# Kernel optimization log

Hardware: AMD Instinct MI355X
Metric: run time of the kernel (lower is better)

## Reference

```python
import jax, jax.numpy as jnp
import numpy as np

D_MODEL, D_STATE, EXPAND = 1024, 16, 2
D_INNER = EXPAND * D_MODEL
BATCH, SEQ = 4, 4096


def setup_inputs() -> dict:
    key = jax.random.key(0)
    ks = jax.random.split(key, 9)
    s = 0.02
    return {
        "x": jax.random.normal(ks[0], (BATCH, SEQ, D_MODEL), jnp.float32),
        # torch Linear weight [out,in] stored transposed here as [in,out]
        "W_in": jax.random.normal(ks[1], (D_MODEL, 2 * D_INNER), jnp.float32) * s,
        "conv_w": jax.random.normal(ks[2], (D_INNER, 1, 3), jnp.float32) * s,  # depthwise, groups=D_INNER
        "conv_b": jax.random.normal(ks[3], (D_INNER,), jnp.float32) * s,
        "W_B": jax.random.normal(ks[4], (D_INNER, D_STATE), jnp.float32) * s,
        "W_C": jax.random.normal(ks[5], (D_INNER, D_STATE), jnp.float32) * s,
        "A": jax.random.normal(ks[6], (D_STATE,), jnp.float32),
        "D": jnp.ones((D_INNER,), jnp.float32),
        "W_out": jax.random.normal(ks[7], (D_INNER, D_MODEL), jnp.float32) * s,
    }


def reference(x, W_in, conv_w, conv_b, W_B, W_C, A, D, W_out):
    d_inner = conv_w.shape[0]
    # input projection and split into main / residual gate paths
    xr = jnp.einsum("bld,de->ble", x, W_in)  # [B, L, 2*d_inner]
    x_main, res = xr[..., :d_inner], xr[..., d_inner:]
    # depthwise conv1d along seq (kernel 3, pad 1)
    xc = jax.lax.conv_general_dilated(
        x_main.transpose(0, 2, 1), conv_w, (1,), [(1, 1)],
        dimension_numbers=("NCH", "OIH", "NCH"), feature_group_count=d_inner)
    xc = (xc + conv_b[None, :, None]).transpose(0, 2, 1)  # [B, L, d_inner]
    xc = jax.nn.silu(xc)
    # selective-scan inputs
    Bt = jnp.einsum("bli,is->bls", xc, W_B)  # [B, L, d_state]
    Ct = jnp.einsum("bli,is->bls", xc, W_C)
    decay = jnp.exp(-jax.nn.softplus(A))  # exp(A_diag), [d_state]

    def step(state, bc):
        b_t, c_t = bc
        state = state * decay + b_t  # i=0: zeros*decay + B[0] == B[0]
        return state, jnp.sum(state * c_t, axis=-1)  # scalar per batch

    _, ys = jax.lax.scan(step, jnp.zeros_like(Bt[:, 0]),
                         (Bt.transpose(1, 0, 2), Ct.transpose(1, 0, 2)))
    ys = ys.T  # [B, L]
    y = ys[..., None] + xc * D  # broadcast scan output across d_inner
    y = y * jax.nn.silu(res)
    return jnp.einsum("bli,id->bld", y, W_out)
```

## Files before the change

kernel.cpp:

```cpp
#include <hip/hip_runtime.h>


typedef _Float16 half8 __attribute__((ext_vector_type(8)));
typedef float floatx4 __attribute__((ext_vector_type(4)));

#define D_MODEL 1024
#define D_INNER 2048
#define SEQ     4096
#define NBATCH  4
#define NROWS   (NBATCH * SEQ)
#define CHUNK   16
#define NCHUNK  (SEQ / CHUNK)
#define NTASK   (NBATCH * NCHUNK)

__device__ __forceinline__ void async16(_Float16* lds, const _Float16* g) {
    __builtin_amdgcn_global_load_lds((const __attribute__((address_space(1))) void*)g,
                                     (__attribute__((address_space(3))) void*)lds, 16, 0, 0);
}

__device__ __forceinline__ float siluf(float x) {
    return x / (1.f + __expf(-x));
}

__device__ __forceinline__ float decay_of(const float* A, int s) {
    return __expf(-log1pf(__expf(A[s])));
}

#define BAR() asm volatile("s_barrier" ::: "memory")


__global__ __launch_bounds__(256) void convert_f32_f16(const float* __restrict__ src,
                                                       _Float16* __restrict__ dst) {
    size_t idx = ((size_t)blockIdx.x * 256 + threadIdx.x) * 8;
    float4 a = *(const float4*)(src + idx);
    float4 b = *(const float4*)(src + idx + 4);
    half8 o = {(_Float16)a.x, (_Float16)a.y, (_Float16)a.z, (_Float16)a.w,
               (_Float16)b.x, (_Float16)b.y, (_Float16)b.z, (_Float16)b.w};
    *(half8*)(dst + idx) = o;
}

__global__ __launch_bounds__(256) void transpose_to_f16(const float* __restrict__ src,
                                                        _Float16* __restrict__ dst,
                                                        int K, int N) {
    __shared__ float tile[32][33];
    int n0 = blockIdx.x * 32, k0 = blockIdx.y * 32;
    int x = threadIdx.x, y = threadIdx.y;
#pragma unroll
    for (int r = 0; r < 32; r += 8)
        tile[y + r][x] = src[(size_t)(k0 + y + r) * N + (n0 + x)];
    __syncthreads();
#pragma unroll
    for (int r = 0; r < 32; r += 8)
        dst[(size_t)(n0 + y + r) * K + (k0 + x)] = (_Float16)tile[x][y + r];
}

__global__ __launch_bounds__(256) void convert_wbct(const float* __restrict__ WB,
                                                    const float* __restrict__ WC,
                                                    _Float16* __restrict__ WBCT) {
    int idx = blockIdx.x * 256 + threadIdx.x;
    int n = idx >> 11, k = idx & 2047;
    float v = (n < 16) ? WB[k * 16 + n] : WC[k * 16 + (n - 16)];
    WBCT[idx] = (_Float16)v;
}


__device__ __forceinline__ void stage_half(const _Float16* __restrict__ src, int K,
                                           int rowBase, int k0, _Float16* ldsHalf) {
    const int tid = threadIdx.x;
    const int sr = tid >> 3, wid = tid >> 6;
    const int lc = ((tid & 7) ^ (sr & 7)) << 3;
#pragma unroll
    for (int r = 0; r < 2; r++) {
        const _Float16* g = src + (size_t)(rowBase + r * 64 + sr) * K + (k0 + lc);
        async16(ldsHalf + r * 4096 + wid * 512, g);
    }
}

__device__ __forceinline__ void loadA8(half8 af[4][2], const _Float16* p,
                                       int sw0, int sw1) {
#pragma unroll
    for (int m = 0; m < 4; m++) {
        af[m][0] = *(const half8*)(p + m * 1024 + sw0);
        af[m][1] = *(const half8*)(p + m * 1024 + sw1);
    }
}

__device__ __forceinline__ void loadB8(half8 bf[4][2], const _Float16* p,
                                       int sw0, int sw1) {
#pragma unroll
    for (int n = 0; n < 4; n++) {
        bf[n][0] = *(const half8*)(p + n * 1024 + sw0);
        bf[n][1] = *(const half8*)(p + n * 1024 + sw1);
    }
}

#define GP_MMA2(CBP)                                                                    \
    BAR();                                                                              \
    __builtin_amdgcn_s_setprio(1);                                                      \
    _Pragma("unroll") for (int s = 0; s < 2; s++)                                       \
        _Pragma("unroll") for (int m = 0; m < 4; m++)                                   \
            _Pragma("unroll") for (int n = 0; n < 4; n++)                               \
                acc[m][(CBP) * 4 + n] = __builtin_amdgcn_mfma_f32_16x16x32_f16(         \
                    af[m][s], bf[n][s], acc[m][(CBP) * 4 + n], 0, 0, 0);                \
    __builtin_amdgcn_s_setprio(0);                                                      \
    BAR();

template <typename OutT, int NC, int RT>
__global__ __launch_bounds__(512, 2) void gemm256(const _Float16* __restrict__ A,
                                                  const _Float16* __restrict__ BT,
                                                  OutT* __restrict__ C,
                                                  int M, int N, int K) {
    __shared__ __align__(16) _Float16 smem[4 * 16384];
    _Float16* const AsBase = smem;
    _Float16* const BsBase = smem + 32768;

    const int tid = threadIdx.x;
    const int wid = tid >> 6, lane = tid & 63;
    const int wm = wid >> 1, wn = wid & 1;
    const int fr = lane & 15, q = lane >> 4, frq = fr & 7;
    const int sw0 = (q ^ frq) << 3;
    const int sw1 = ((4 + q) ^ frq) << 3;
    const int aB0 = (wm * 64 + fr) * 64;
    const int bB0 = (wn * 128 + fr) * 64;

    const int b = blockIdx.x;
    const int col0 = (b % NC) * 256;
    const int rowBase = (b / NC) * (RT * 256);
    const int NT = K >> 6;

    half8 af[4][2], bf[4][2];

    stage_half(A,  K, rowBase,       0, AsBase);
    stage_half(A,  K, rowBase + 128, 0, AsBase + 8192);
    stage_half(BT, K, col0,          0, BsBase);
    stage_half(BT, K, col0 + 128,    0, BsBase + 8192);
    stage_half(A,  K, rowBase,      64, AsBase + 16384);
    asm volatile("s_waitcnt vmcnt(2)" ::: "memory");
    BAR();

    for (int rt = 0; rt < RT; ++rt) {
        const int row0 = rowBase + rt * 256;
        floatx4 acc[4][8] = {};

        for (int t = 0; t < NT; ++t) {
            _Float16* Ab  = AsBase + ((t & 1) << 14);
            _Float16* Bb  = BsBase + ((t & 1) << 14);
            _Float16* Abn = AsBase + (((t + 1) & 1) << 14);
            _Float16* Bbn = BsBase + (((t + 1) & 1) << 14);
            const int k1 = (t + 1) << 6, k2 = (t + 2) << 6;
            const bool s1 = (t + 1) < NT, s2 = (t + 2) < NT;

            loadA8(af, Ab + aB0, sw0, sw1);
            loadB8(bf, Bb + bB0, sw0, sw1);
            if (s1) {
                stage_half(A,  K, row0 + 128, k1, Abn + 8192);
                stage_half(BT, K, col0,       k1, Bbn);
            }
            GP_MMA2(0);

            loadB8(bf, Bb + bB0 + 4096, sw0, sw1);
            if (s1) stage_half(BT, K, col0 + 128, k1, Bbn + 8192);
            if (s2) stage_half(A, K, row0, k2, Ab);
            if (s2) {
                asm volatile("s_waitcnt vmcnt(2)" ::: "memory");
            } else if (s1) {
                asm volatile("s_waitcnt vmcnt(0)" ::: "memory");
            }
            GP_MMA2(1);
        }

        const int er = (lane >> 4) * 4, ec = lane & 15;
#pragma unroll
        for (int mi = 0; mi < 4; mi++)
#pragma unroll
            for (int cj = 0; cj < 8; cj++)
#pragma unroll
                for (int r = 0; r < 4; r++) {
                    int row = row0 + wm * 64 + mi * 16 + er + r;
                    int col = col0 + wn * 128 + cj * 16 + ec;
                    C[(size_t)row * N + col] = (OutT)acc[mi][cj][r];
                }

        if (rt + 1 < RT) {
            const int row0n = row0 + 256;
            stage_half(A,  K, row0n,       0, AsBase);
            stage_half(A,  K, row0n + 128, 0, AsBase + 8192);
            stage_half(BT, K, col0,        0, BsBase);
            stage_half(BT, K, col0 + 128,  0, BsBase + 8192);
            stage_half(A,  K, row0n,      64, AsBase + 16384);
            asm volatile("s_waitcnt vmcnt(2)" ::: "memory");
            BAR();
        }
    }
}

__global__ __launch_bounds__(256) void conv_bc_fin(const _Float16* __restrict__ xr,
                                                   const float* __restrict__ cw,
                                                   const float* __restrict__ cb,
                                                   const _Float16* __restrict__ WBCT,
                                                   const float* __restrict__ A,
                                                   _Float16* __restrict__ xc,
                                                   float* __restrict__ BtCt,
                                                   float* __restrict__ fin) {
    __shared__ __align__(16) _Float16 As[4 * 32 * 128];
    const int tid = threadIdx.x, wid = tid >> 6, lane = tid & 63;
    const int row0 = blockIdx.x * 32;
    const int l0 = row0 & (SEQ - 1);
    const int cg = lane & 15;
    const int rg = lane >> 4;
    const int fr = lane & 15, q = lane >> 4;
    _Float16* As_w = As + wid * 4096;
    const int r0 = rg * 8;

    floatx4 acc[2][2] = {};

    for (int t = 0; t < 4; t++) {
        const int kbase = wid * 512 + t * 128;
        const int gcol = kbase + cg * 8;
        float w0[8], w1[8], w2[8], bb[8];
#pragma unroll
        for (int j = 0; j < 8; j++) {
            w0[j] = cw[(gcol + j) * 3];
            w1[j] = cw[(gcol + j) * 3 + 1];
            w2[j] = cw[(gcol + j) * 3 + 2];
            bb[j] = cb[gcol + j];
        }
        half8 prev = {}, cur, nxt;
        if (!(l0 == 0 && rg == 0))
            prev = *(const half8*)(xr + (size_t)(row0 + r0 - 1) * 4096 + gcol);
        cur = *(const half8*)(xr + (size_t)(row0 + r0) * 4096 + gcol);
#pragma unroll
        for (int r = 0; r < 8; r++) {
            if (r == 7 && rg == 3 && l0 + 32 == SEQ) {
                half8 z = {};
                nxt = z;
            } else {
                nxt = *(const half8*)(xr + (size_t)(row0 + r0 + r + 1) * 4096 + gcol);
            }
            half8 o;
#pragma unroll
            for (int j = 0; j < 8; j++) {
                float a = (float)prev[j] * w0[j] + (float)cur[j] * w1[j] +
                          (float)nxt[j] * w2[j] + bb[j];
                o[j] = (_Float16)siluf(a);
            }
            const int lrow = r0 + r;
            *(half8*)(xc + (size_t)(row0 + lrow) * D_INNER + gcol) = o;
            *(half8*)(As_w + lrow * 128 + ((cg ^ (lrow & 7)) * 8)) = o;
            prev = cur;
            cur = nxt;
        }
#pragma unroll
        for (int ks = 0; ks < 4; ks++) {
            half8 af[2], bf[2];
#pragma unroll
            for (int rt = 0; rt < 2; rt++)
                af[rt] = *(const half8*)(As_w + (rt * 16 + fr) * 128 +
                                         (((ks * 4 + q) ^ (fr & 7)) * 8));
#pragma unroll
            for (int ot = 0; ot < 2; ot++)
                bf[ot] = *(const half8*)(WBCT + (size_t)(ot * 16 + fr) * D_INNER +
                                         kbase + ks * 32 + q * 8);
#pragma unroll
            for (int rt = 0; rt < 2; rt++)
#pragma unroll
                for (int ot = 0; ot < 2; ot++)
                    acc[rt][ot] = __builtin_amdgcn_mfma_f32_16x16x32_f16(af[rt], bf[ot], acc[rt][ot], 0, 0, 0);
        }
    }

    __syncthreads();
    float* red = (float*)As;
    float* btl = (float*)As + 4096;
    const int er = (lane >> 4) * 4, ec = lane & 15;
#pragma unroll
    for (int rt = 0; rt < 2; rt++)
#pragma unroll
        for (int ot = 0; ot < 2; ot++)
#pragma unroll
            for (int rr = 0; rr < 4; rr++)
                red[wid * 1024 + (rt * 16 + er + rr) * 32 + ot * 16 + ec] = acc[rt][ot][rr];
    __syncthreads();
#pragma unroll
    for (int i = 0; i < 4; i++) {
        int idx = i * 256 + tid;
        float v = red[idx] + red[1024 + idx] + red[2048 + idx] + red[3072 + idx];
        btl[idx] = v;
        BtCt[(size_t)row0 * 32 + idx] = v;
    }
    __syncthreads();
    if (tid < 32) {
        const int ch = tid >> 4, s = tid & 15;
        const float decay = decay_of(A, s);
        float st = 0.f;
#pragma unroll
        for (int r = 0; r < CHUNK; r++)
            st = st * decay + btl[(ch * 16 + r) * 32 + s];
        fin[((row0 >> 4) + ch) * 16 + s] = st;
    }
}

__global__ __launch_bounds__(64) void scan_p2(const float* __restrict__ fin,
                                              const float* __restrict__ A,
                                              float* __restrict__ carry) {
    int t = threadIdx.x;
    int b = t >> 4, s = t & 15;
    float decay = decay_of(A, s);
    float d16 = decay;
#pragma unroll
    for (int k = 0; k < 4; k++) d16 *= d16;
    float cy = 0.f;
#pragma unroll 8
    for (int c = 0; c < NCHUNK; c++) {
        int idx = ((b * NCHUNK) + c) * 16 + s;
        carry[idx] = cy;
        cy = cy * d16 + fin[idx];
    }
}

__global__ __launch_bounds__(256) void scan_p3_fuse(const float* __restrict__ BtCt,
                                                    const float* __restrict__ A,
                                                    const float* __restrict__ carry,
                                                    const float* __restrict__ D,
                                                    const _Float16* __restrict__ xr,
                                                    _Float16* __restrict__ xc) {
    __shared__ float ysl[CHUNK];
    const int task = blockIdx.x;
    const int b = task >> 8, c = task & (NCHUNK - 1);
    const int row0 = b * SEQ + c * CHUNK;
    const int tid = threadIdx.x;

    if (tid < 16) {
        const int s = tid;
        const float decay = decay_of(A, s);
        size_t r = (size_t)row0 * 32;
        float bt[CHUNK], ct[CHUNK];
#pragma unroll
        for (int j = 0; j < CHUNK; j++) {
            bt[j] = BtCt[r + (size_t)j * 32 + s];
            ct[j] = BtCt[r + (size_t)j * 32 + 16 + s];
        }
        float st = carry[task * 16 + s];
        float yv[CHUNK];
#pragma unroll
        for (int j = 0; j < CHUNK; j++) {
            st = st * decay + bt[j];
            yv[j] = st * ct[j];
        }
#pragma unroll
        for (int j = 0; j < CHUNK; j++) {
            float y = yv[j];
            y += __shfl_xor(y, 1, 16);
            y += __shfl_xor(y, 2, 16);
            y += __shfl_xor(y, 4, 16);
            y += __shfl_xor(y, 8, 16);
            if (s == 0) ysl[j] = y;
        }
    }
    __syncthreads();

#pragma unroll
    for (int it = 0; it < 16; it++) {
        int chunk = it * 256 + tid;
        int rl = chunk >> 8;
        int colb = (chunk & 255) * 8;
        size_t row = (size_t)(row0 + rl);
        float yv = ysl[rl];
        half8 x8 = *(const half8*)(xc + row * D_INNER + colb);
        half8 r8 = *(const half8*)(xr + row * 4096 + 2048 + colb);
        float4 d0 = *(const float4*)(D + colb);
        float4 d1 = *(const float4*)(D + colb + 4);
        half8 o;
        float dd[8] = {d0.x, d0.y, d0.z, d0.w, d1.x, d1.y, d1.z, d1.w};
#pragma unroll
        for (int j = 0; j < 8; j++) {
            float y = yv + (float)x8[j] * dd[j];
            o[j] = (_Float16)(y * siluf((float)r8[j]));
        }
        *(half8*)(xc + row * D_INNER + colb) = o;
    }
}

extern "C" void kernel_launch(void* const* d_in, const int* in_sizes, int n_in,
                              void* d_out, int out_size, void* d_ws, size_t ws_size,
                              hipStream_t stream) {
    const float* x      = (const float*)d_in[0];
    const float* W_in   = (const float*)d_in[1];
    const float* conv_w = (const float*)d_in[2];
    const float* conv_b = (const float*)d_in[3];
    const float* W_B    = (const float*)d_in[4];
    const float* W_C    = (const float*)d_in[5];
    const float* A      = (const float*)d_in[6];
    const float* D      = (const float*)d_in[7];
    const float* W_out  = (const float*)d_in[8];
    float* out = (float*)d_out;

    char* ws = (char*)d_ws;
    size_t off = 0;
    auto alloc = [&](size_t bytes) { size_t o = off; off += (bytes + 255) & ~(size_t)255; return o; };
    _Float16* xh    = (_Float16*)(ws + alloc((size_t)NROWS * D_MODEL * 2));
    _Float16* WinT  = (_Float16*)(ws + alloc((size_t)4096 * 1024 * 2));
    _Float16* WoutT = (_Float16*)(ws + alloc((size_t)1024 * 2048 * 2));
    _Float16* WBCT  = (_Float16*)(ws + alloc((size_t)32 * 2048 * 2));
    _Float16* xr    = (_Float16*)(ws + alloc((size_t)NROWS * 4096 * 2));
    _Float16* xc    = (_Float16*)(ws + alloc((size_t)NROWS * D_INNER * 2));
    float*    BtCt  = (float*)(ws + alloc((size_t)NROWS * 32 * 4));
    float*    fin   = (float*)(ws + alloc((size_t)NTASK * 16 * 4));
    float*    carry = (float*)(ws + alloc((size_t)NTASK * 16 * 4));

    convert_f32_f16<<<(NROWS * D_MODEL) / (256 * 8), 256, 0, stream>>>(x, xh);
    transpose_to_f16<<<dim3(4096 / 32, 1024 / 32), dim3(32, 8), 0, stream>>>(W_in, WinT, 1024, 4096);
    transpose_to_f16<<<dim3(1024 / 32, 2048 / 32), dim3(32, 8), 0, stream>>>(W_out, WoutT, 2048, 1024);
    convert_wbct<<<(32 * 2048) / 256, 256, 0, stream>>>(W_B, W_C, WBCT);
    gemm256<_Float16, 16, 4><<<256, 512, 0, stream>>>(xh, WinT, xr, NROWS, 4096, 1024);
    conv_bc_fin<<<NROWS / 32, 256, 0, stream>>>(xr, conv_w, conv_b, WBCT, A, xc, BtCt, fin);
    scan_p2<<<1, 64, 0, stream>>>(fin, A, carry);
    scan_p3_fuse<<<NTASK, 256, 0, stream>>>(BtCt, A, carry, D, xr, xc);
    gemm256<float, 4, 1><<<256, 512, 0, stream>>>(xc, WoutT, out, NROWS, 1024, 2048);
}
```

Baseline: 450.3 us.

## Switch GEMM inner product from 16x16x32 to 32x32x16 MFMA tiles

Replaces the 16x16x32 f16 MFMA fragments with 32x32x16 MFMA, so each wave holds a 2x4 grid of 32x32 accumulators instead of a 4x8 grid of 16x16. Fragment loads from LDS and the output epilogue are rewritten to match the new lane-to-row/column mapping. The goal is fewer LDS fragment reads per FLOP and fewer MFMA issues. The trade-off is a different LDS bank-access pattern under the existing swizzle and a less coalesced epilogue store layout. A leftover unused loadA32 helper with convoluted indexing is also added.

```diff
diff --git a/kernel.cpp b/kernel.cpp
--- a/kernel.cpp
+++ b/kernel.cpp
@@ -3,6 +3,7 @@
 
 typedef _Float16 half8 __attribute__((ext_vector_type(8)));
 typedef float floatx4 __attribute__((ext_vector_type(4)));
+typedef float floatx16 __attribute__((ext_vector_type(16)));
 
 #define D_MODEL 1024
 #define D_INNER 2048
@@ -76,32 +77,28 @@
     }
 }
 
-__device__ __forceinline__ void loadA8(half8 af[4][2], const _Float16* p,
-                                       int sw0, int sw1) {
-#pragma unroll
-    for (int m = 0; m < 4; m++) {
-        af[m][0] = *(const half8*)(p + m * 1024 + sw0);
-        af[m][1] = *(const half8*)(p + m * 1024 + sw1);
-    }
-}
-
-__device__ __forceinline__ void loadB8(half8 bf[4][2], const _Float16* p,
-                                       int sw0, int sw1) {
-#pragma unroll
-    for (int n = 0; n < 4; n++) {
-        bf[n][0] = *(const half8*)(p + n * 1024 + sw0);
-        bf[n][1] = *(const half8*)(p + n * 1024 + sw1);
-    }
-}
-
-#define GP_MMA2(CBP)                                                                    \
+__device__ __forceinline__ void loadA32(half8 af[2][2], const _Float16* Ab,
+                                        int rowBase, int rowXor, int kb, int hk) {
+#pragma unroll
+    for (int m = 0; m < 2; m++) {
+        const int row = rowBase + m * 32;
+#pragma unroll
+        for (int kkl = 0; kkl < 2; kkl++) {
+            const int c = (kb + kkl) * 2 + hk;
+            af[m][kkl] = *(const half8*)(Ab + row * 64 + (((c ^ rowXor) ^ ((row & 7) ^ rowXor)) << 3)
+                                         + ((c ^ (row & 7)) - ((c ^ rowXor) ^ ((row & 7) ^ rowXor))) * 0);
+        }
+    }
+}
+
+#define GP_MMA32(AF, BF)                                                                \
     BAR();                                                                              \
     __builtin_amdgcn_s_setprio(1);                                                      \
-    _Pragma("unroll") for (int s = 0; s < 2; s++)                                       \
-        _Pragma("unroll") for (int m = 0; m < 4; m++)                                   \
+    _Pragma("unroll") for (int kkl = 0; kkl < 2; kkl++)                                 \
+        _Pragma("unroll") for (int m = 0; m < 2; m++)                                   \
             _Pragma("unroll") for (int n = 0; n < 4; n++)                               \
-                acc[m][(CBP) * 4 + n] = __builtin_amdgcn_mfma_f32_16x16x32_f16(         \
-                    af[m][s], bf[n][s], acc[m][(CBP) * 4 + n], 0, 0, 0);                \
+                acc[m][n] = __builtin_amdgcn_mfma_f32_32x32x16_f16(                     \
+                    (AF)[m][kkl], (BF)[n][kkl], acc[m][n], 0, 0, 0);                    \
     __builtin_amdgcn_s_setprio(0);                                                      \
     BAR();
 
@@ -117,18 +114,16 @@
     const int tid = threadIdx.x;
     const int wid = tid >> 6, lane = tid & 63;
     const int wm = wid >> 1, wn = wid & 1;
-    const int fr = lane & 15, q = lane >> 4, frq = fr & 7;
-    const int sw0 = (q ^ frq) << 3;
-    const int sw1 = ((4 + q) ^ frq) << 3;
-    const int aB0 = (wm * 64 + fr) * 64;
-    const int bB0 = (wn * 128 + fr) * 64;
+    const int r32 = lane & 31, hk = lane >> 5;
+    const int aRow0 = wm * 64 + r32;
+    const int bRow0 = wn * 128 + r32;
 
     const int b = blockIdx.x;
     const int col0 = (b % NC) * 256;
     const int rowBase = (b / NC) * (RT * 256);
     const int NT = K >> 6;
 
-    half8 af[4][2], bf[4][2];
+    half8 af[2][2], bf[4][2];
 
     stage_half(A,  K, rowBase,       0, AsBase);
     stage_half(A,  K, rowBase + 128, 0, AsBase + 8192);
@@ -140,7 +135,7 @@
 
     for (int rt = 0; rt < RT; ++rt) {
         const int row0 = rowBase + rt * 256;
-        floatx4 acc[4][8] = {};
+        floatx16 acc[2][4] = {};
 
         for (int t = 0; t < NT; ++t) {
             _Float16* Ab  = AsBase + ((t & 1) << 14);
@@ -150,15 +145,48 @@
             const int k1 = (t + 1) << 6, k2 = (t + 2) << 6;
             const bool s1 = (t + 1) < NT, s2 = (t + 2) < NT;
 
-            loadA8(af, Ab + aB0, sw0, sw1);
-            loadB8(bf, Bb + bB0, sw0, sw1);
+#pragma unroll
+            for (int m = 0; m < 2; m++) {
+                const int row = aRow0 + m * 32;
+#pragma unroll
+                for (int kkl = 0; kkl < 2; kkl++) {
+                    const int c = kkl * 2 + hk;
+                    af[m][kkl] = *(const half8*)(Ab + row * 64 + ((c ^ (row & 7)) << 3));
+                }
+            }
+#pragma unroll
+            for (int n = 0; n < 4; n++) {
+                const int row = bRow0 + n * 32;
+#pragma unroll
+                for (int kkl = 0; kkl < 2; kkl++) {
+                    const int c = kkl * 2 + hk;
+                    bf[n][kkl] = *(const half8*)(Bb + row * 64 + ((c ^ (row & 7)) << 3));
+                }
+            }
             if (s1) {
                 stage_half(A,  K, row0 + 128, k1, Abn + 8192);
                 stage_half(BT, K, col0,       k1, Bbn);
             }
-            GP_MMA2(0);
-
-            loadB8(bf, Bb + bB0 + 4096, sw0, sw1);
+            GP_MMA32(af, bf);
+
+#pragma unroll
+            for (int m = 0; m < 2; m++) {
+                const int row = aRow0 + m * 32;
+#pragma unroll
+                for (int kkl = 0; kkl < 2; kkl++) {
+                    const int c = (2 + kkl) * 2 + hk;
+                    af[m][kkl] = *(const half8*)(Ab + row * 64 + ((c ^ (row & 7)) << 3));
+                }
+            }
+#pragma unroll
+            for (int n = 0; n < 4; n++) {
+                const int row = bRow0 + n * 32;
+#pragma unroll
+                for (int kkl = 0; kkl < 2; kkl++) {
+                    const int c = (2 + kkl) * 2 + hk;
+                    bf[n][kkl] = *(const half8*)(Bb + row * 64 + ((c ^ (row & 7)) << 3));
+                }
+            }
             if (s1) stage_half(BT, K, col0 + 128, k1, Bbn + 8192);
             if (s2) stage_half(A, K, row0, k2, Ab);
             if (s2) {
@@ -166,19 +194,18 @@
             } else if (s1) {
                 asm volatile("s_waitcnt vmcnt(0)" ::: "memory");
             }
-            GP_MMA2(1);
-        }
-
-        const int er = (lane >> 4) * 4, ec = lane & 15;
-#pragma unroll
-        for (int mi = 0; mi < 4; mi++)
-#pragma unroll
-            for (int cj = 0; cj < 8; cj++)
-#pragma unroll
-                for (int r = 0; r < 4; r++) {
-                    int row = row0 + wm * 64 + mi * 16 + er + r;
-                    int col = col0 + wn * 128 + cj * 16 + ec;
-                    C[(size_t)row * N + col] = (OutT)acc[mi][cj][r];
+            GP_MMA32(af, bf);
+        }
+
+#pragma unroll
+        for (int m = 0; m < 2; m++)
+#pragma unroll
+            for (int n = 0; n < 4; n++)
+#pragma unroll
+                for (int reg = 0; reg < 16; reg++) {
+                    int row = row0 + wm * 64 + m * 32 + (reg & 3) + 8 * (reg >> 2) + 4 * hk;
+                    int col = col0 + wn * 128 + n * 32 + r32;
+                    C[(size_t)row * N + col] = (OutT)acc[m][n][reg];
                 }
 
         if (rt + 1 < RT) {
```

New measurement: 466.0 us. +3.5%, slower.
